# Kernel optimization log

Measured on AMD Instinct MI355X. Metric: run time of the kernel, lower is better.

The kernel has to match this reference:

```python
import jax, jax.numpy as jnp
import numpy as np

B, C, N, M = 128, 1024, 8192, 128  # batch, controller_size, memory_units, key_size(=memory_unit_size)
EPS = 1e-16


def setup_inputs() -> dict:
    key = jax.random.key(0)
    ks = jax.random.split(key, 16)
    controller_state = jax.random.normal(ks[0], (B, C), dtype=jnp.float32)
    pw = jax.random.uniform(ks[1], (B, N), dtype=jnp.float32)
    prev_weights = pw / jnp.sum(pw, axis=1, keepdims=True)  # valid attention distribution
    memory = jax.random.normal(ks[2], (B, N, M), dtype=jnp.float32)
    sc = 0.02
    params = {
        "Wk": sc * jax.random.normal(ks[3], (C, M), dtype=jnp.float32), "bk": jnp.zeros((M,), jnp.float32),
        "Wb": sc * jax.random.normal(ks[4], (C, 1), dtype=jnp.float32), "bb": jnp.zeros((1,), jnp.float32),
        "Wg": sc * jax.random.normal(ks[5], (C, 1), dtype=jnp.float32), "bg": jnp.zeros((1,), jnp.float32),
        "Ws": sc * jax.random.normal(ks[6], (C, 3), dtype=jnp.float32), "bs": jnp.zeros((3,), jnp.float32),
        "Wy": sc * jax.random.normal(ks[7], (C, 1), dtype=jnp.float32), "by": jnp.zeros((1,), jnp.float32),
        "Wa": sc * jax.random.normal(ks[8], (C, M), dtype=jnp.float32), "ba": jnp.zeros((M,), jnp.float32),
    }
    return {"controller_state": controller_state, "prev_weights": prev_weights, "memory": memory, **params}


def reference(controller_state, prev_weights, memory, Wk, bk, Wb, bb, Wg, bg, Ws, bs, Wy, by, Wa, ba):
    cs = controller_state
    k = cs @ Wk + bk                                    # (B, M) key
    beta = jax.nn.softplus(cs @ Wb + bb)                # (B, 1) key strength
    g = jax.nn.sigmoid(cs @ Wg + bg)                    # (B, 1) interpolation gate
    s = jax.nn.softmax(cs @ Ws + bs, axis=1)            # (B, 3) shift weighting
    y = 1.0 + jax.nn.softplus(cs @ Wy + by)             # (B, 1) sharpen factor
    # content addressing: softmax(beta * cosine_sim(key, memory rows))
    dots = jnp.einsum("bnm,bm->bn", memory, k)          # (B, N)
    mnorm = jnp.linalg.norm(memory, axis=2)             # (B, N)
    knorm = jnp.linalg.norm(k, axis=1, keepdims=True)   # (B, 1)
    cos = dots / (mnorm * knorm + EPS)
    content_weights = jax.nn.softmax(beta * cos, axis=1)
    # interpolate with previous weights
    iw = g * content_weights + (1.0 - g) * prev_weights
    # circular 3-tap shift: c[i] = s0*w[i-1] + s1*w[i] + s2*w[i+1] (circular)
    sw = (s[:, 0:1] * jnp.roll(iw, 1, axis=1)
          + s[:, 1:2] * iw
          + s[:, 2:3] * jnp.roll(iw, -1, axis=1))
    # sharpen + normalize
    w = sw ** y
    w = w / (jnp.sum(w, axis=1, keepdims=True) + EPS)
    # read mode: data = w @ memory
    data = jnp.einsum("bn,bnm->bm", w, memory)          # (B, M)
    return (w, data)
```

## Files before the change

### kernel.cpp

```cpp
#include <hip/hip_runtime.h>
#include <math.h>

#define Bsz 128
#define Csz 1024
#define Nsz 8192
#define Msz 128
#define EPSF 1e-16f

__device__ __forceinline__ float softplusf(float x) {
    return (x > 20.f) ? x : log1pf(expf(x));
}

__global__ __launch_bounds__(128) void kA(
    const float* __restrict__ cs,
    const float* __restrict__ Wk, const float* __restrict__ bk,
    const float* __restrict__ Wb, const float* __restrict__ bb,
    const float* __restrict__ Wg, const float* __restrict__ bg,
    const float* __restrict__ Ws, const float* __restrict__ bs,
    const float* __restrict__ Wy, const float* __restrict__ by,
    float* __restrict__ K, float* __restrict__ scal)
{
    const int b = blockIdx.x;
    const int t = threadIdx.x;
    __shared__ float lcs[Csz];
    __shared__ float red[128];

    #pragma unroll
    for (int j = 0; j < Csz / 128; ++j) lcs[t + j * 128] = cs[b * Csz + t + j * 128];
    __syncthreads();

    float ka = 0.f;
    #pragma unroll 4
    for (int c = 0; c < Csz; ++c) ka += lcs[c] * Wk[c * Msz + t];
    ka += bk[t];
    K[b * Msz + t] = ka;

    float ab = 0.f, ag = 0.f, ay = 0.f, a0 = 0.f, a1 = 0.f, a2 = 0.f;
    for (int c = t; c < Csz; c += 128) {
        float v = lcs[c];
        ab += v * Wb[c];
        ag += v * Wg[c];
        ay += v * Wy[c];
        a0 += v * Ws[c * 3 + 0];
        a1 += v * Ws[c * 3 + 1];
        a2 += v * Ws[c * 3 + 2];
    }

    auto redu = [&](float v) -> float {
        __syncthreads();
        red[t] = v;
        __syncthreads();
        for (int off = 64; off > 0; off >>= 1) {
            if (t < off) red[t] += red[t + off];
            __syncthreads();
        }
        return red[0];
    };

    float db = redu(ab);
    float dg = redu(ag);
    float dy = redu(ay);
    float d0 = redu(a0);
    float d1 = redu(a1);
    float d2 = redu(a2);
    float dq = redu(ka * ka);

    if (t == 0) {
        float beta = softplusf(db + bb[0]);
        float g = 1.f / (1.f + expf(-(dg + bg[0])));
        float yv = 1.f + softplusf(dy + by[0]);
        float l0 = d0 + bs[0], l1 = d1 + bs[1], l2 = d2 + bs[2];
        float m3 = fmaxf(l0, fmaxf(l1, l2));
        float e0 = expf(l0 - m3), e1 = expf(l1 - m3), e2 = expf(l2 - m3);
        float inv = 1.f / (e0 + e1 + e2);
        scal[b * 8 + 0] = sqrtf(dq);
        scal[b * 8 + 1] = beta;
        scal[b * 8 + 2] = g;
        scal[b * 8 + 3] = e0 * inv;
        scal[b * 8 + 4] = e1 * inv;
        scal[b * 8 + 5] = e2 * inv;
        scal[b * 8 + 6] = yv;
    }
}

__global__ __launch_bounds__(256) void kB(
    const float* __restrict__ mem, const float* __restrict__ K,
    const float* __restrict__ scal, float* __restrict__ z)
{
    const int b = blockIdx.x >> 7;
    const int n0 = (blockIdx.x & 127) * 64;
    const int t = threadIdx.x;
    const int rl = t & 15, rg = t >> 4;

    __shared__ float lk[Msz];
    if (t < Msz) lk[t] = K[b * Msz + t];
    __syncthreads();

    const float knorm = scal[b * 8 + 0];
    const float beta = scal[b * 8 + 1];

    const float k0 = lk[rl * 4 + 0], k1 = lk[rl * 4 + 1];
    const float k2 = lk[rl * 4 + 2], k3 = lk[rl * 4 + 3];
    const float k4 = lk[64 + rl * 4 + 0], k5 = lk[64 + rl * 4 + 1];
    const float k6 = lk[64 + rl * 4 + 2], k7 = lk[64 + rl * 4 + 3];

    const float* base = mem + (size_t)b * Nsz * Msz;

    #pragma unroll
    for (int i = 0; i < 4; ++i) {
        const int n = n0 + i * 16 + rg;
        const float4* p = (const float4*)(base + (size_t)n * Msz);
        float4 a = p[rl];
        float4 c = p[16 + rl];
        float dot = a.x * k0 + a.y * k1 + a.z * k2 + a.w * k3
                  + c.x * k4 + c.y * k5 + c.z * k6 + c.w * k7;
        float sq = a.x * a.x + a.y * a.y + a.z * a.z + a.w * a.w
                 + c.x * c.x + c.y * c.y + c.z * c.z + c.w * c.w;
        #pragma unroll
        for (int off = 8; off; off >>= 1) {
            dot += __shfl_xor(dot, off, 16);
            sq  += __shfl_xor(sq,  off, 16);
        }
        if (rl == 0) {
            float mn = sqrtf(sq);
            float cosv = dot / (mn * knorm + EPSF);
            z[(size_t)b * Nsz + n] = beta * cosv;
        }
    }
}

__global__ __launch_bounds__(256) void kC(
    const float* __restrict__ z, float* __restrict__ stats)
{
    const int b = blockIdx.x, t = threadIdx.x;
    const float* zb = z + (size_t)b * Nsz;
    __shared__ float red[256];

    float mx = -1e30f;
    for (int i = t; i < Nsz; i += 256) mx = fmaxf(mx, zb[i]);
    red[t] = mx;
    __syncthreads();
    for (int off = 128; off; off >>= 1) {
        if (t < off) red[t] = fmaxf(red[t], red[t + off]);
        __syncthreads();
    }
    mx = red[0];
    __syncthreads();

    float s = 0.f;
    for (int i = t; i < Nsz; i += 256) s += expf(zb[i] - mx);
    red[t] = s;
    __syncthreads();
    for (int off = 128; off; off >>= 1) {
        if (t < off) red[t] += red[t + off];
        __syncthreads();
    }
    if (t == 0) { stats[b * 2 + 0] = mx; stats[b * 2 + 1] = red[0]; }
}

__global__ __launch_bounds__(256) void kD(
    const float* __restrict__ z, const float* __restrict__ pw,
    const float* __restrict__ scal, const float* __restrict__ stats,
    float* __restrict__ tbuf, float* __restrict__ S)
{
    const int gid = blockIdx.x * 256 + threadIdx.x;
    const int b = gid >> 13;
    const int n = gid & (Nsz - 1);

    const float mx = stats[b * 2 + 0];
    const float invl = 1.f / stats[b * 2 + 1];
    const float g = scal[b * 8 + 2];
    const float s0 = scal[b * 8 + 3], s1 = scal[b * 8 + 4], s2 = scal[b * 8 + 5];
    const float yv = scal[b * 8 + 6];

    const int nm1 = (n == 0) ? Nsz - 1 : n - 1;
    const int np1 = (n == Nsz - 1) ? 0 : n + 1;
    const size_t bo = (size_t)b * Nsz;

    const float om = 1.f - g;
    float iwm = g * (expf(z[bo + nm1] - mx) * invl) + om * pw[bo + nm1];
    float iw0 = g * (expf(z[bo + n  ] - mx) * invl) + om * pw[bo + n  ];
    float iwp = g * (expf(z[bo + np1] - mx) * invl) + om * pw[bo + np1];

    float sw = s0 * iwm + s1 * iw0 + s2 * iwp;
    float tv = powf(sw, yv);
    tbuf[bo + n] = tv;

    __shared__ float red[256];
    red[threadIdx.x] = tv;
    __syncthreads();
    for (int off = 128; off; off >>= 1) {
        if (threadIdx.x < off) red[threadIdx.x] += red[threadIdx.x + off];
        __syncthreads();
    }
    if (threadIdx.x == 0) atomicAdd(&S[b], red[0]);
}

__global__ __launch_bounds__(256) void kE(
    const float* __restrict__ mem, const float* __restrict__ tbuf,
    const float* __restrict__ S, float* __restrict__ wout,
    float* __restrict__ dacc)
{
    const int b = blockIdx.x >> 6;
    const int n0 = (blockIdx.x & 63) * 128;
    const int t = threadIdx.x;
    const int rl = t & 15, rg = t >> 4;

    const float invS = 1.f / (S[b] + EPSF);
    const float* base = mem + (size_t)b * Nsz * Msz;
    const float* tb = tbuf + (size_t)b * Nsz;

    float acc[8] = {0.f, 0.f, 0.f, 0.f, 0.f, 0.f, 0.f, 0.f};

    #pragma unroll
    for (int i = 0; i < 8; ++i) {
        const int n = n0 + i * 16 + rg;
        const float tv = tb[n];
        const float4* p = (const float4*)(base + (size_t)n * Msz);
        float4 a = p[rl];
        float4 c = p[16 + rl];
        acc[0] += tv * a.x; acc[1] += tv * a.y; acc[2] += tv * a.z; acc[3] += tv * a.w;
        acc[4] += tv * c.x; acc[5] += tv * c.y; acc[6] += tv * c.z; acc[7] += tv * c.w;
        if (rl == 0) wout[(size_t)b * Nsz + n] = tv * invS;
    }

    __shared__ float red[256 * 8];
    #pragma unroll
    for (int j = 0; j < 8; ++j) red[t * 8 + j] = acc[j];
    __syncthreads();

    if (t < Msz) {
        const int half = t >> 6, rl2 = (t & 63) >> 2, jj = t & 3;
        float s = 0.f;
        #pragma unroll
        for (int gq = 0; gq < 16; ++gq) s += red[(gq * 16 + rl2) * 8 + half * 4 + jj];
        atomicAdd(&dacc[b * Msz + t], s);
    }
}

__global__ __launch_bounds__(256) void kF(
    const float* __restrict__ dacc, const float* __restrict__ S,
    float* __restrict__ dout)
{
    const int gid = blockIdx.x * 256 + threadIdx.x;
    if (gid < Bsz * Msz) {
        const int b = gid >> 7;
        dout[gid] = dacc[gid] / (S[b] + EPSF);
    }
}

extern "C" void kernel_launch(void* const* d_in, const int* in_sizes, int n_in,
                              void* d_out, int out_size, void* d_ws, size_t ws_size,
                              hipStream_t stream) {
    const float* cs  = (const float*)d_in[0];
    const float* pw  = (const float*)d_in[1];
    const float* mem = (const float*)d_in[2];
    const float* Wk  = (const float*)d_in[3];
    const float* bk  = (const float*)d_in[4];
    const float* Wb  = (const float*)d_in[5];
    const float* bb  = (const float*)d_in[6];
    const float* Wg  = (const float*)d_in[7];
    const float* bg  = (const float*)d_in[8];
    const float* Ws  = (const float*)d_in[9];
    const float* bs  = (const float*)d_in[10];
    const float* Wy  = (const float*)d_in[11];
    const float* by  = (const float*)d_in[12];

    float* out = (float*)d_out;
    float* wout = out;
    float* dout = out + (size_t)Bsz * Nsz;

    float* wsf   = (float*)d_ws;
    float* K     = wsf;
    float* scal  = K + Bsz * Msz;
    float* stats = scal + Bsz * 8;
    float* S     = stats + Bsz * 2;
    float* dacc  = S + Bsz;
    float* z     = dacc + Bsz * Msz;
    float* tbuf  = z + (size_t)Bsz * Nsz;

    hipMemsetAsync(S, 0, (size_t)(Bsz + Bsz * Msz) * sizeof(float), stream);

    kA<<<Bsz, 128, 0, stream>>>(cs, Wk, bk, Wb, bb, Wg, bg, Ws, bs, Wy, by, K, scal);
    kB<<<Bsz * (Nsz / 64), 256, 0, stream>>>(mem, K, scal, z);
    kC<<<Bsz, 256, 0, stream>>>(z, stats);
    kD<<<(Bsz * Nsz) / 256, 256, 0, stream>>>(z, pw, scal, stats, tbuf, S);
    kE<<<Bsz * (Nsz / 128), 256, 0, stream>>>(mem, tbuf, S, wout, dacc);
    kF<<<(Bsz * Msz + 255) / 256, 256, 0, stream>>>(dacc, S, dout);
}
```

Baseline: 953.5 us.

## Fuse softmax denominator into cosine kernel, drop max pass, split key GEMV

The separate softmax-statistics kernel is removed. The cosine-similarity kernel now accumulates exp(z) per batch with an atomic add, which relies on |beta*cos| being bounded so no max subtraction is needed. kA splits the C reduction across two 128-thread halves, kD replaces powf with exp(y*log), and kE walks its blocks in reverse so the memory tail kB touched last may still be in cache. The trade-off is an extra atomic per block and overflow risk if beta grows large.

```diff
diff --git a/kernel.cpp b/kernel.cpp
--- a/kernel.cpp
+++ b/kernel.cpp
@@ -11,7 +11,7 @@
     return (x > 20.f) ? x : log1pf(expf(x));
 }
 
-__global__ __launch_bounds__(128) void kA(
+__global__ __launch_bounds__(256) void kA(
     const float* __restrict__ cs,
     const float* __restrict__ Wk, const float* __restrict__ bk,
     const float* __restrict__ Wb, const float* __restrict__ bb,
@@ -22,21 +22,23 @@
 {
     const int b = blockIdx.x;
     const int t = threadIdx.x;
+    const int m = t & 127, h = t >> 7;
     __shared__ float lcs[Csz];
-    __shared__ float red[128];
-
-    #pragma unroll
-    for (int j = 0; j < Csz / 128; ++j) lcs[t + j * 128] = cs[b * Csz + t + j * 128];
+    __shared__ float kpart[256];
+    __shared__ float red[256];
+
+    #pragma unroll
+    for (int j = 0; j < Csz / 256; ++j) lcs[t + j * 256] = cs[b * Csz + t + j * 256];
     __syncthreads();
 
     float ka = 0.f;
-    #pragma unroll 4
-    for (int c = 0; c < Csz; ++c) ka += lcs[c] * Wk[c * Msz + t];
-    ka += bk[t];
-    K[b * Msz + t] = ka;
+    const int c0 = h * (Csz / 2);
+    #pragma unroll 8
+    for (int c = c0; c < c0 + Csz / 2; ++c) ka += lcs[c] * Wk[c * Msz + m];
+    kpart[t] = ka;
 
     float ab = 0.f, ag = 0.f, ay = 0.f, a0 = 0.f, a1 = 0.f, a2 = 0.f;
-    for (int c = t; c < Csz; c += 128) {
+    for (int c = t; c < Csz; c += 256) {
         float v = lcs[c];
         ab += v * Wb[c];
         ag += v * Wg[c];
@@ -45,12 +47,19 @@
         a1 += v * Ws[c * 3 + 1];
         a2 += v * Ws[c * 3 + 2];
     }
+    __syncthreads();
+
+    float kfull = 0.f;
+    if (h == 0) {
+        kfull = kpart[m] + kpart[128 + m] + bk[m];
+        K[b * Msz + m] = kfull;
+    }
 
     auto redu = [&](float v) -> float {
         __syncthreads();
         red[t] = v;
         __syncthreads();
-        for (int off = 64; off > 0; off >>= 1) {
+        for (int off = 128; off > 0; off >>= 1) {
             if (t < off) red[t] += red[t + off];
             __syncthreads();
         }
@@ -63,7 +72,7 @@
     float d0 = redu(a0);
     float d1 = redu(a1);
     float d2 = redu(a2);
-    float dq = redu(ka * ka);
+    float dq = redu(kfull * kfull);
 
     if (t == 0) {
         float beta = softplusf(db + bb[0]);
@@ -85,7 +94,8 @@
 
 __global__ __launch_bounds__(256) void kB(
     const float* __restrict__ mem, const float* __restrict__ K,
-    const float* __restrict__ scal, float* __restrict__ z)
+    const float* __restrict__ scal, float* __restrict__ z,
+    float* __restrict__ sumexp)
 {
     const int b = blockIdx.x >> 7;
     const int n0 = (blockIdx.x & 127) * 64;
@@ -93,6 +103,7 @@
     const int rl = t & 15, rg = t >> 4;
 
     __shared__ float lk[Msz];
+    __shared__ float lred[16];
     if (t < Msz) lk[t] = K[b * Msz + t];
     __syncthreads();
 
@@ -106,6 +117,7 @@
 
     const float* base = mem + (size_t)b * Nsz * Msz;
 
+    float ez = 0.f;
     #pragma unroll
     for (int i = 0; i < 4; ++i) {
         const int n = n0 + i * 16 + rg;
@@ -123,52 +135,31 @@
         }
         if (rl == 0) {
             float mn = sqrtf(sq);
-            float cosv = dot / (mn * knorm + EPSF);
-            z[(size_t)b * Nsz + n] = beta * cosv;
+            float zv = beta * (dot / (mn * knorm + EPSF));
+            z[(size_t)b * Nsz + n] = zv;
+            ez += expf(zv);
         }
     }
-}
-
-__global__ __launch_bounds__(256) void kC(
-    const float* __restrict__ z, float* __restrict__ stats)
-{
-    const int b = blockIdx.x, t = threadIdx.x;
-    const float* zb = z + (size_t)b * Nsz;
-    __shared__ float red[256];
-
-    float mx = -1e30f;
-    for (int i = t; i < Nsz; i += 256) mx = fmaxf(mx, zb[i]);
-    red[t] = mx;
-    __syncthreads();
-    for (int off = 128; off; off >>= 1) {
-        if (t < off) red[t] = fmaxf(red[t], red[t + off]);
-        __syncthreads();
-    }
-    mx = red[0];
-    __syncthreads();
-
-    float s = 0.f;
-    for (int i = t; i < Nsz; i += 256) s += expf(zb[i] - mx);
-    red[t] = s;
-    __syncthreads();
-    for (int off = 128; off; off >>= 1) {
-        if (t < off) red[t] += red[t + off];
-        __syncthreads();
-    }
-    if (t == 0) { stats[b * 2 + 0] = mx; stats[b * 2 + 1] = red[0]; }
+    if (rl == 0) lred[rg] = ez;
+    __syncthreads();
+    if (t == 0) {
+        float s = 0.f;
+        #pragma unroll
+        for (int j = 0; j < 16; ++j) s += lred[j];
+        atomicAdd(&sumexp[b], s);
+    }
 }
 
 __global__ __launch_bounds__(256) void kD(
     const float* __restrict__ z, const float* __restrict__ pw,
-    const float* __restrict__ scal, const float* __restrict__ stats,
+    const float* __restrict__ scal, const float* __restrict__ sumexp,
     float* __restrict__ tbuf, float* __restrict__ S)
 {
     const int gid = blockIdx.x * 256 + threadIdx.x;
     const int b = gid >> 13;
     const int n = gid & (Nsz - 1);
 
-    const float mx = stats[b * 2 + 0];
-    const float invl = 1.f / stats[b * 2 + 1];
+    const float invl = 1.f / sumexp[b];
     const float g = scal[b * 8 + 2];
     const float s0 = scal[b * 8 + 3], s1 = scal[b * 8 + 4], s2 = scal[b * 8 + 5];
     const float yv = scal[b * 8 + 6];
@@ -178,12 +169,12 @@
     const size_t bo = (size_t)b * Nsz;
 
     const float om = 1.f - g;
-    float iwm = g * (expf(z[bo + nm1] - mx) * invl) + om * pw[bo + nm1];
-    float iw0 = g * (expf(z[bo + n  ] - mx) * invl) + om * pw[bo + n  ];
-    float iwp = g * (expf(z[bo + np1] - mx) * invl) + om * pw[bo + np1];
+    float iwm = g * (expf(z[bo + nm1]) * invl) + om * pw[bo + nm1];
+    float iw0 = g * (expf(z[bo + n  ]) * invl) + om * pw[bo + n  ];
+    float iwp = g * (expf(z[bo + np1]) * invl) + om * pw[bo + np1];
 
     float sw = s0 * iwm + s1 * iw0 + s2 * iwp;
-    float tv = powf(sw, yv);
+    float tv = expf(yv * logf(sw));
     tbuf[bo + n] = tv;
 
     __shared__ float red[256];
@@ -201,8 +192,9 @@
     const float* __restrict__ S, float* __restrict__ wout,
     float* __restrict__ dacc)
 {
-    const int b = blockIdx.x >> 6;
-    const int n0 = (blockIdx.x & 63) * 128;
+    const int ridx = (int)gridDim.x - 1 - (int)blockIdx.x;
+    const int b = ridx >> 6;
+    const int n0 = (ridx & 63) * 128;
     const int t = threadIdx.x;
     const int rl = t & 15, rg = t >> 4;
 
@@ -270,21 +262,20 @@
     float* wout = out;
     float* dout = out + (size_t)Bsz * Nsz;
 
-    float* wsf   = (float*)d_ws;
-    float* K     = wsf;
-    float* scal  = K + Bsz * Msz;
-    float* stats = scal + Bsz * 8;
-    float* S     = stats + Bsz * 2;
-    float* dacc  = S + Bsz;
-    float* z     = dacc + Bsz * Msz;
-    float* tbuf  = z + (size_t)Bsz * Nsz;
-
-    hipMemsetAsync(S, 0, (size_t)(Bsz + Bsz * Msz) * sizeof(float), stream);
-
-    kA<<<Bsz, 128, 0, stream>>>(cs, Wk, bk, Wb, bb, Wg, bg, Ws, bs, Wy, by, K, scal);
-    kB<<<Bsz * (Nsz / 64), 256, 0, stream>>>(mem, K, scal, z);
-    kC<<<Bsz, 256, 0, stream>>>(z, stats);
-    kD<<<(Bsz * Nsz) / 256, 256, 0, stream>>>(z, pw, scal, stats, tbuf, S);
+    float* wsf    = (float*)d_ws;
+    float* K      = wsf;
+    float* scal   = K + Bsz * Msz;
+    float* S      = scal + Bsz * 8;
+    float* sumexp = S + Bsz;
+    float* dacc   = sumexp + Bsz;
+    float* z      = dacc + Bsz * Msz;
+    float* tbuf   = z + (size_t)Bsz * Nsz;
+
+    hipMemsetAsync(S, 0, (size_t)(Bsz + Bsz + Bsz * Msz) * sizeof(float), stream);
+
+    kA<<<Bsz, 256, 0, stream>>>(cs, Wk, bk, Wb, bb, Wg, bg, Ws, bs, Wy, by, K, scal);
+    kB<<<Bsz * (Nsz / 64), 256, 0, stream>>>(mem, K, scal, z, sumexp);
+    kD<<<(Bsz * Nsz) / 256, 256, 0, stream>>>(z, pw, scal, sumexp, tbuf, S);
     kE<<<Bsz * (Nsz / 128), 256, 0, stream>>>(mem, tbuf, S, wout, dacc);
     kF<<<(Bsz * Msz + 255) / 256, 256, 0, stream>>>(dacc, S, dout);
 }
```

After: 871.2 us. -8.6%, faster.
